# Kernel tuning notes

Measured on AMD Instinct MI355X. Metric: run time of the kernel, lower is better.

## Reference

```python
import jax, jax.numpy as jnp
import numpy as np

N_NODES = 50000
N_GRAPHS = 500
NODES_PER_GRAPH = 100
N_EDGES = 800000
D_IN = 64
D_H = 64


def setup_inputs() -> dict:
    key = jax.random.key(0)
    ks = jax.random.split(key, 12)
    s_in = 1.0 / np.sqrt(D_IN)
    s_h = 1.0 / np.sqrt(D_H)
    x = jax.random.normal(ks[0], (N_NODES, D_IN), jnp.float32)
    edge_index = jax.random.randint(ks[1], (2, N_EDGES), 0, N_NODES, dtype=jnp.int32)
    # 500 graphs of exactly 100 nodes each (sorted segment ids)
    batch = jnp.repeat(jnp.arange(N_GRAPHS, dtype=jnp.int32), NODES_PER_GRAPH)
    center_pos = jax.random.randint(ks[2], (N_GRAPHS,), 0, NODES_PER_GRAPH, dtype=jnp.int32)
    return {
        "x": x,
        "edge_index": edge_index,
        "batch": batch,
        "center_pos": center_pos,
        "Wl1": jax.random.normal(ks[3], (D_H, D_IN), jnp.float32) * s_in,
        "bl1": jax.random.normal(ks[4], (D_H,), jnp.float32) * s_in,
        "Wr1": jax.random.normal(ks[5], (D_H, D_IN), jnp.float32) * s_in,
        "Wl2": jax.random.normal(ks[6], (D_H, D_H), jnp.float32) * s_h,
        "bl2": jax.random.normal(ks[7], (D_H,), jnp.float32) * s_h,
        "Wr2": jax.random.normal(ks[8], (D_H, D_H), jnp.float32) * s_h,
        "Wlin": jax.random.normal(ks[9], (1, D_H), jnp.float32) * s_h,
        "blin": jax.random.normal(ks[10], (1,), jnp.float32) * s_h,
    }


def _sage_conv(x, src, dst, Wl, bl, Wr):
    # mean-aggregate source features onto target nodes, then
    # out = lin_l(mean_agg) + lin_r(x)  (PyG SAGEConv, aggr='mean')
    msg = x[src]                                              # [E, d] gather
    agg = jax.ops.segment_sum(msg, dst, num_segments=N_NODES)  # [N, d]
    deg = jax.ops.segment_sum(jnp.ones((src.shape[0],), x.dtype), dst,
                              num_segments=N_NODES)            # [N]
    mean = agg / jnp.maximum(deg, 1.0)[:, None]
    return mean @ Wl.T + bl + x @ Wr.T


def reference(x, edge_index, batch, center_pos, Wl1, bl1, Wr1, Wl2, bl2, Wr2, Wlin, blin):
    src, dst = edge_index[0], edge_index[1]
    h = jax.nn.relu(_sage_conv(x, src, dst, Wl1, bl1, Wr1))
    h = jax.nn.relu(_sage_conv(h, src, dst, Wl2, bl2, Wr2))
    # gather-based readout of center node per graph
    counts = jnp.bincount(batch, length=N_GRAPHS)              # [G]
    offsets = jnp.cumsum(counts) - counts                      # [G]
    center_global = offsets + center_pos.reshape(-1)           # [G]
    x_center = h[center_global]                                # [G, d]
    out = (x_center @ Wlin.T + blin).squeeze(-1)               # [G]
    return out
```

## Files before the change

### kernel.cpp

```cpp
#include <hip/hip_runtime.h>


constexpr int NN  = 50000;
constexpr int NG  = 500;
constexpr int NPG = 100;
constexpr int NE  = 800000;
constexpr int D   = 64;


__global__ void k_init(const int* __restrict__ cpos, int* __restrict__ flag) {
  int g = blockIdx.x * blockDim.x + threadIdx.x;
  if (g < NG) {
    int c = g * NPG + cpos[g];
    flag[c] = 3;
  }
}

__global__ void k_mark(const int* __restrict__ src, const int* __restrict__ dst,
                       int* __restrict__ flag, int* __restrict__ deg) {
  int stride = gridDim.x * blockDim.x;
  for (int e = blockIdx.x * blockDim.x + threadIdx.x; e < NE; e += stride) {
    int d = dst[e];
    atomicAdd(&deg[d], 1);
    if (flag[d] & 1) atomicOr(&flag[src[e]], 2);
  }
}

template <int BIT>
__global__ void k_agg(const int* __restrict__ src, const int* __restrict__ dst,
                      const int* __restrict__ flag, const float* __restrict__ feat,
                      float* __restrict__ agg) {
  int lane = threadIdx.x & 63;
  int wid  = (blockIdx.x * blockDim.x + threadIdx.x) >> 6;
  int nw   = (gridDim.x * blockDim.x) >> 6;
  for (int base = wid * 64; base < NE; base += nw * 64) {
    int e = base + lane;
    int s = 0, d = 0;
    bool m = false;
    if (e < NE) {
      d = dst[e];
      m = (flag[d] & BIT) != 0;
      if (m) s = src[e];
    }
    unsigned long long bal = __ballot(m);
    while (bal) {
      int b = __ffsll(bal) - 1;
      bal &= bal - 1;
      int sd = __shfl(s, b);
      int dd = __shfl(d, b);
      float v = feat[sd * D + lane];
      if (BIT == 1)
        atomicAdd(&agg[(dd / NPG) * D + lane], v);
      else
        atomicAdd(&agg[dd * D + lane], v);
    }
  }
}

__global__ void k_sage1(const float* __restrict__ x, const int* __restrict__ flag,
                        const int* __restrict__ deg, float* __restrict__ agg1,
                        const float* __restrict__ Wl, const float* __restrict__ bl,
                        const float* __restrict__ Wr) {
  __shared__ float sWl[D * 65];
  __shared__ float sWr[D * 65];
  __shared__ float sbl[D];
  int tid = threadIdx.x;
  for (int i = tid; i < D * D; i += blockDim.x) {
    int r = i >> 6, c = i & 63;
    sWl[r * 65 + c] = Wl[i];
    sWr[r * 65 + c] = Wr[i];
  }
  if (tid < D) sbl[tid] = bl[tid];
  __syncthreads();

  int lane = tid & 63;
  int wid  = (blockIdx.x * blockDim.x + tid) >> 6;
  int nw   = (gridDim.x * blockDim.x) >> 6;
  for (int v = wid; v < NN; v += nw) {
    if (!(flag[v] & 2)) continue;
    float dg = (float)deg[v];
    if (dg < 1.f) dg = 1.f;
    float m  = agg1[v * D + lane] / dg;
    float xv = x[v * D + lane];
    float h  = sbl[lane];
#pragma unroll
    for (int k = 0; k < D; k++) {
      float mk = __shfl(m, k);
      float xk = __shfl(xv, k);
      h += sWl[lane * 65 + k] * mk + sWr[lane * 65 + k] * xk;
    }
    agg1[v * D + lane] = fmaxf(h, 0.f);
  }
}

__global__ void k_final(const float* __restrict__ h1, const float* __restrict__ agg2,
                        const int* __restrict__ deg, const int* __restrict__ cpos,
                        const float* __restrict__ Wl2, const float* __restrict__ bl2,
                        const float* __restrict__ Wr2, const float* __restrict__ Wlin,
                        const float* __restrict__ blin, float* __restrict__ out) {
  int lane = threadIdx.x & 63;
  int g = (blockIdx.x * blockDim.x + threadIdx.x) >> 6;
  if (g >= NG) return;
  int c = g * NPG + cpos[g];
  float dg = (float)deg[c];
  if (dg < 1.f) dg = 1.f;
  float m  = agg2[g * D + lane] / dg;
  float hc = h1[c * D + lane];
  float h  = bl2[lane];
#pragma unroll
  for (int k = 0; k < D; k++) {
    h += Wl2[lane * D + k] * __shfl(m, k) + Wr2[lane * D + k] * __shfl(hc, k);
  }
  h = fmaxf(h, 0.f);
  float p = Wlin[lane] * h;
#pragma unroll
  for (int off = 32; off; off >>= 1) p += __shfl_down(p, off);
  if (lane == 0) out[g] = p + blin[0];
}

extern "C" void kernel_launch(void* const* d_in, const int* in_sizes, int n_in,
                              void* d_out, int out_size, void* d_ws, size_t ws_size,
                              hipStream_t stream) {
  const float* x    = (const float*)d_in[0];
  const int*   ei   = (const int*)d_in[1];
  const int*   srcI = ei;
  const int*   dstI = ei + NE;
  const int*   cpos = (const int*)d_in[3];
  const float* Wl1  = (const float*)d_in[4];
  const float* bl1  = (const float*)d_in[5];
  const float* Wr1  = (const float*)d_in[6];
  const float* Wl2  = (const float*)d_in[7];
  const float* bl2  = (const float*)d_in[8];
  const float* Wr2  = (const float*)d_in[9];
  const float* Wlin = (const float*)d_in[10];
  const float* blin = (const float*)d_in[11];
  float* out = (float*)d_out;

  char* ws = (char*)d_ws;
  float* agg1 = (float*)ws;
  float* agg2 = (float*)(ws + (size_t)NN * D * 4);
  int*   deg  = (int*)(ws + (size_t)NN * D * 4 + (size_t)NG * D * 4);
  int*   flag = deg + NN;
  size_t total = (size_t)NN * D * 4 + (size_t)NG * D * 4 + (size_t)NN * 4 * 2;

  hipMemsetAsync(d_ws, 0, total, stream);
  k_init<<<2, 256, 0, stream>>>(cpos, flag);
  k_mark<<<2048, 256, 0, stream>>>(srcI, dstI, flag, deg);
  k_agg<2><<<2048, 256, 0, stream>>>(srcI, dstI, flag, x, agg1);
  k_sage1<<<1024, 256, 0, stream>>>(x, flag, deg, agg1, Wl1, bl1, Wr1);
  k_agg<1><<<2048, 256, 0, stream>>>(srcI, dstI, flag, agg1, agg2);
  k_final<<<(NG * 64 + 255) / 256, 256, 0, stream>>>(agg1, agg2, deg, cpos,
                                                     Wl2, bl2, Wr2, Wlin, blin, out);
}
```

Baseline: 212.5 us.

## Compact receptive-field nodes and record center edges to skip full passes

Nodes needed for the center readouts are compacted into dense slots, so the aggregation buffer shrinks from all nodes to a fixed capacity and the large zeroing memset of the full per-node buffer goes away. Degree counting moves into the filtered aggregation, so only needed nodes get degree atomics. Edges into center nodes are recorded during marking, so the second-layer aggregation walks a short edge list instead of rescanning all edges. Fixed capacities (16384 slots and edges) rely on the receptive field staying small; entries beyond capacity are silently dropped.

```diff
diff --git a/kernel.cpp b/kernel.cpp
--- a/kernel.cpp
+++ b/kernel.cpp
@@ -6,61 +6,108 @@
 constexpr int NPG = 100;
 constexpr int NE  = 800000;
 constexpr int D   = 64;
+constexpr int SCAP = 16384;
+constexpr int ECAP = 16384;
+
+constexpr size_t OFF_AGGC  = 0;
+constexpr size_t OFF_AGG2  = OFF_AGGC + (size_t)SCAP * D * 4;
+constexpr size_t OFF_FLAG  = OFF_AGG2 + (size_t)NG * D * 4;
+constexpr size_t OFF_DEGC  = OFF_FLAG + (size_t)NN * 4;
+constexpr size_t OFF_CNT   = OFF_DEGC + (size_t)SCAP * 4;
+constexpr size_t OFF_NODE  = OFF_CNT + 16;
+constexpr size_t OFF_ELIST = OFF_NODE + (size_t)SCAP * 4;
+constexpr size_t MEMSET_BYTES = OFF_NODE - OFF_AGG2;
 
 
 __global__ void k_init(const int* __restrict__ cpos, int* __restrict__ flag) {
   int g = blockIdx.x * blockDim.x + threadIdx.x;
-  if (g < NG) {
-    int c = g * NPG + cpos[g];
-    flag[c] = 3;
-  }
+  if (g < NG) flag[g * NPG + cpos[g]] = 3;
 }
 
 __global__ void k_mark(const int* __restrict__ src, const int* __restrict__ dst,
-                       int* __restrict__ flag, int* __restrict__ deg) {
-  int stride = gridDim.x * blockDim.x;
-  for (int e = blockIdx.x * blockDim.x + threadIdx.x; e < NE; e += stride) {
-    int d = dst[e];
-    atomicAdd(&deg[d], 1);
-    if (flag[d] & 1) atomicOr(&flag[src[e]], 2);
-  }
-}
-
-template <int BIT>
-__global__ void k_agg(const int* __restrict__ src, const int* __restrict__ dst,
-                      const int* __restrict__ flag, const float* __restrict__ feat,
-                      float* __restrict__ agg) {
+                       int* __restrict__ flag, int2* __restrict__ elist,
+                       int* __restrict__ cnt) {
   int lane = threadIdx.x & 63;
   int wid  = (blockIdx.x * blockDim.x + threadIdx.x) >> 6;
   int nw   = (gridDim.x * blockDim.x) >> 6;
   for (int base = wid * 64; base < NE; base += nw * 64) {
     int e = base + lane;
-    int s = 0, d = 0;
-    bool m = false;
-    if (e < NE) {
-      d = dst[e];
-      m = (flag[d] & BIT) != 0;
-      if (m) s = src[e];
-    }
+    int d = dst[e];
+    bool m = (flag[d] & 1) != 0;
+    int s = 0;
+    if (m) s = src[e];
+    unsigned long long bal = __ballot(m);
+    if (m) atomicOr(&flag[s], 2);
+    int n = __popcll(bal);
+    if (n) {
+      int basei;
+      if (lane == 0) basei = atomicAdd(&cnt[0], n);
+      basei = __shfl(basei, 0);
+      if (m) {
+        int idx = basei + __popcll(bal & ((1ull << lane) - 1));
+        if (idx < ECAP) elist[idx] = make_int2(s, d);
+      }
+    }
+  }
+}
+
+__global__ void k_compact(int* __restrict__ flag, int* __restrict__ nodelist,
+                          float* __restrict__ aggC, int* __restrict__ cnt) {
+  int v = blockIdx.x * blockDim.x + threadIdx.x;
+  int lane = threadIdx.x & 63;
+  bool m = false;
+  int f = 0;
+  if (v < NN) { f = flag[v]; m = (f & 2) != 0; }
+  unsigned long long bal = __ballot(m);
+  int n = __popcll(bal);
+  if (n) {
+    int basei;
+    if (lane == 0) basei = atomicAdd(&cnt[1], n);
+    basei = __shfl(basei, 0);
+    if (m) {
+      int slot = basei + __popcll(bal & ((1ull << lane) - 1));
+      if (slot < SCAP) {
+        flag[v] = f | (slot << 2);
+        nodelist[slot] = v;
+        float4 z = make_float4(0.f, 0.f, 0.f, 0.f);
+        float4* row = (float4*)&aggC[(size_t)slot * D];
+#pragma unroll
+        for (int i = 0; i < D / 4; i++) row[i] = z;
+      }
+    }
+  }
+}
+
+__global__ void k_agg2(const int* __restrict__ src, const int* __restrict__ dst,
+                       const int* __restrict__ flag, const float* __restrict__ x,
+                       float* __restrict__ aggC, int* __restrict__ degC) {
+  int lane = threadIdx.x & 63;
+  int wid  = (blockIdx.x * blockDim.x + threadIdx.x) >> 6;
+  int nw   = (gridDim.x * blockDim.x) >> 6;
+  for (int base = wid * 64; base < NE; base += nw * 64) {
+    int e = base + lane;
+    int d = dst[e];
+    int f = flag[d];
+    bool m = (f & 2) != 0;
+    int s = 0;
+    if (m) s = src[e];
     unsigned long long bal = __ballot(m);
     while (bal) {
       int b = __ffsll(bal) - 1;
       bal &= bal - 1;
-      int sd = __shfl(s, b);
-      int dd = __shfl(d, b);
-      float v = feat[sd * D + lane];
-      if (BIT == 1)
-        atomicAdd(&agg[(dd / NPG) * D + lane], v);
-      else
-        atomicAdd(&agg[dd * D + lane], v);
-    }
-  }
-}
-
-__global__ void k_sage1(const float* __restrict__ x, const int* __restrict__ flag,
-                        const int* __restrict__ deg, float* __restrict__ agg1,
+      int ss = __shfl(s, b);
+      int sl = __shfl(f, b) >> 2;
+      float v = x[(size_t)ss * D + lane];
+      atomicAdd(&aggC[(size_t)sl * D + lane], v);
+      if (lane == 0) atomicAdd(&degC[sl], 1);
+    }
+  }
+}
+
+__global__ void k_sage1(const float* __restrict__ x, const int* __restrict__ nodelist,
+                        const int* __restrict__ degC, float* __restrict__ aggC,
                         const float* __restrict__ Wl, const float* __restrict__ bl,
-                        const float* __restrict__ Wr) {
+                        const float* __restrict__ Wr, const int* __restrict__ cnt) {
   __shared__ float sWl[D * 65];
   __shared__ float sWr[D * 65];
   __shared__ float sbl[D];
@@ -73,39 +120,57 @@
   if (tid < D) sbl[tid] = bl[tid];
   __syncthreads();
 
+  int scnt = cnt[1];
+  if (scnt > SCAP) scnt = SCAP;
   int lane = tid & 63;
   int wid  = (blockIdx.x * blockDim.x + tid) >> 6;
   int nw   = (gridDim.x * blockDim.x) >> 6;
-  for (int v = wid; v < NN; v += nw) {
-    if (!(flag[v] & 2)) continue;
-    float dg = (float)deg[v];
+  for (int slot = wid; slot < scnt; slot += nw) {
+    int v = nodelist[slot];
+    float dg = (float)degC[slot];
     if (dg < 1.f) dg = 1.f;
-    float m  = agg1[v * D + lane] / dg;
-    float xv = x[v * D + lane];
+    float m  = aggC[(size_t)slot * D + lane] / dg;
+    float xv = x[(size_t)v * D + lane];
     float h  = sbl[lane];
 #pragma unroll
     for (int k = 0; k < D; k++) {
-      float mk = __shfl(m, k);
-      float xk = __shfl(xv, k);
-      h += sWl[lane * 65 + k] * mk + sWr[lane * 65 + k] * xk;
-    }
-    agg1[v * D + lane] = fmaxf(h, 0.f);
-  }
-}
-
-__global__ void k_final(const float* __restrict__ h1, const float* __restrict__ agg2,
-                        const int* __restrict__ deg, const int* __restrict__ cpos,
-                        const float* __restrict__ Wl2, const float* __restrict__ bl2,
-                        const float* __restrict__ Wr2, const float* __restrict__ Wlin,
-                        const float* __restrict__ blin, float* __restrict__ out) {
+      h += sWl[lane * 65 + k] * __shfl(m, k) + sWr[lane * 65 + k] * __shfl(xv, k);
+    }
+    aggC[(size_t)slot * D + lane] = fmaxf(h, 0.f);
+  }
+}
+
+__global__ void k_agg1(const int2* __restrict__ elist, const int* __restrict__ flag,
+                       const float* __restrict__ aggC, float* __restrict__ agg2,
+                       const int* __restrict__ cnt) {
+  int ecnt = cnt[0];
+  if (ecnt > ECAP) ecnt = ECAP;
+  int lane = threadIdx.x & 63;
+  int wid  = (blockIdx.x * blockDim.x + threadIdx.x) >> 6;
+  int nw   = (gridDim.x * blockDim.x) >> 6;
+  for (int i = wid; i < ecnt; i += nw) {
+    int2 ed = elist[i];
+    int sl = flag[ed.x] >> 2;
+    int g  = ed.y / NPG;
+    atomicAdd(&agg2[(size_t)g * D + lane], aggC[(size_t)sl * D + lane]);
+  }
+}
+
+__global__ void k_final(const float* __restrict__ aggC, const float* __restrict__ agg2,
+                        const int* __restrict__ degC, const int* __restrict__ flag,
+                        const int* __restrict__ cpos, const float* __restrict__ Wl2,
+                        const float* __restrict__ bl2, const float* __restrict__ Wr2,
+                        const float* __restrict__ Wlin, const float* __restrict__ blin,
+                        float* __restrict__ out) {
   int lane = threadIdx.x & 63;
   int g = (blockIdx.x * blockDim.x + threadIdx.x) >> 6;
   if (g >= NG) return;
-  int c = g * NPG + cpos[g];
-  float dg = (float)deg[c];
+  int c  = g * NPG + cpos[g];
+  int sl = flag[c] >> 2;
+  float dg = (float)degC[sl];
   if (dg < 1.f) dg = 1.f;
-  float m  = agg2[g * D + lane] / dg;
-  float hc = h1[c * D + lane];
+  float m  = agg2[(size_t)g * D + lane] / dg;
+  float hc = aggC[(size_t)sl * D + lane];
   float h  = bl2[lane];
 #pragma unroll
   for (int k = 0; k < D; k++) {
@@ -137,18 +202,21 @@
   float* out = (float*)d_out;
 
   char* ws = (char*)d_ws;
-  float* agg1 = (float*)ws;
-  float* agg2 = (float*)(ws + (size_t)NN * D * 4);
-  int*   deg  = (int*)(ws + (size_t)NN * D * 4 + (size_t)NG * D * 4);
-  int*   flag = deg + NN;
-  size_t total = (size_t)NN * D * 4 + (size_t)NG * D * 4 + (size_t)NN * 4 * 2;
-
-  hipMemsetAsync(d_ws, 0, total, stream);
+  float* aggC = (float*)(ws + OFF_AGGC);
+  float* agg2 = (float*)(ws + OFF_AGG2);
+  int*   flag = (int*)(ws + OFF_FLAG);
+  int*   degC = (int*)(ws + OFF_DEGC);
+  int*   cnt  = (int*)(ws + OFF_CNT);
+  int*   nlst = (int*)(ws + OFF_NODE);
+  int2*  elst = (int2*)(ws + OFF_ELIST);
+
+  hipMemsetAsync(ws + OFF_AGG2, 0, MEMSET_BYTES, stream);
   k_init<<<2, 256, 0, stream>>>(cpos, flag);
-  k_mark<<<2048, 256, 0, stream>>>(srcI, dstI, flag, deg);
-  k_agg<2><<<2048, 256, 0, stream>>>(srcI, dstI, flag, x, agg1);
-  k_sage1<<<1024, 256, 0, stream>>>(x, flag, deg, agg1, Wl1, bl1, Wr1);
-  k_agg<1><<<2048, 256, 0, stream>>>(srcI, dstI, flag, agg1, agg2);
-  k_final<<<(NG * 64 + 255) / 256, 256, 0, stream>>>(agg1, agg2, deg, cpos,
+  k_mark<<<2048, 256, 0, stream>>>(srcI, dstI, flag, elst, cnt);
+  k_compact<<<(NN + 255) / 256, 256, 0, stream>>>(flag, nlst, aggC, cnt);
+  k_agg2<<<2048, 256, 0, stream>>>(srcI, dstI, flag, x, aggC, degC);
+  k_sage1<<<512, 256, 0, stream>>>(x, nlst, degC, aggC, Wl1, bl1, Wr1, cnt);
+  k_agg1<<<256, 256, 0, stream>>>(elst, flag, aggC, agg2, cnt);
+  k_final<<<(NG * 64 + 255) / 256, 256, 0, stream>>>(aggC, agg2, degC, flag, cpos,
                                                      Wl2, bl2, Wr2, Wlin, blin, out);
 }
```

After: 255.0 us. +20.0%, slower.
